# Kernel optimization log

Measured on AMD Instinct MI355X. Metric: run time of the kernel, lower is better.

Reference implementation:

```python
import jax, jax.numpy as jnp
import numpy as np

B, C, N = 8, 256, 4096
CQK = C // 4  # 64
BN_EPS = 1e-5


def setup_inputs() -> dict:
    key = jax.random.key(0)
    ks = jax.random.split(key, 10)
    s = 1.0 / np.sqrt(C)
    return {
        "x": jax.random.normal(ks[0], (B, C, N), jnp.float32),
        "xyz": jax.random.normal(ks[1], (B, C, N), jnp.float32),
        # q_conv and k_conv share the same weight/bias in the original module
        "wqk": jax.random.uniform(ks[2], (CQK, C), jnp.float32, -s, s),
        "bqk": jax.random.uniform(ks[3], (CQK,), jnp.float32, -s, s),
        "wv": jax.random.uniform(ks[4], (C, C), jnp.float32, -s, s),
        "bv": jax.random.uniform(ks[5], (C,), jnp.float32, -s, s),
        "wt": jax.random.uniform(ks[6], (C, C), jnp.float32, -s, s),
        "bt": jax.random.uniform(ks[7], (C,), jnp.float32, -s, s),
        "bn_gamma": jnp.ones((C,), jnp.float32),
        "bn_beta": jnp.zeros((C,), jnp.float32),
        "bn_mean": jax.random.normal(ks[8], (C,), jnp.float32) * 0.1,
        "bn_var": jax.random.uniform(ks[9], (C,), jnp.float32, 0.5, 1.5),
    }


def _conv1x1(x, w, b):
    # x: [B, Cin, N], w: [Cout, Cin], b: [Cout] -> [B, Cout, N]
    return jnp.einsum('oc,bcn->bon', w, x) + b[None, :, None]


def reference(x, xyz, wqk, bqk, wv, bv, wt, bt, bn_gamma, bn_beta, bn_mean, bn_var):
    x = x + xyz
    q = _conv1x1(x, wqk, bqk)            # [B, 64, N]
    k = _conv1x1(x, wqk, bqk)            # [B, 64, N] (shared weights)
    v = _conv1x1(x, wv, bv)              # [B, C, N]
    energy = jnp.einsum('bci,bcj->bij', q, k)   # q^T k -> [B, N, N]
    attn = jax.nn.softmax(energy, axis=-1)
    attn = attn / (1e-9 + attn.sum(axis=1, keepdims=True))  # L1 column renorm
    x_r = jnp.einsum('bcn,bnm->bcm', v, attn)    # [B, C, N]
    t = _conv1x1(x - x_r, wt, bt)
    # BatchNorm1d (eval mode, running stats)
    inv = jax.lax.rsqrt(bn_var + BN_EPS)
    t = (t - bn_mean[None, :, None]) * (inv * bn_gamma)[None, :, None] + bn_beta[None, :, None]
    x_r = jnp.where(t >= 0, t, 0.2 * t)          # LeakyReLU(0.2)
    return x + x_r
```

## Files before the change

### kernel.cpp

```cpp
#include <hip/hip_runtime.h>
#include <math.h>

#define B_   8
#define C_   256
#define N_   4096
#define CQK_ 64
#define JS_  8
#define NSPLIT 2
#define NRANGE (N_ / NSPLIT)

#define SCQ 1.20110674f
#define THR2 11.54f

typedef __attribute__((ext_vector_type(8))) short short8v;
typedef __attribute__((ext_vector_type(4))) short short4v;
typedef __attribute__((ext_vector_type(4))) float f32x4;
typedef __attribute__((ext_vector_type(16))) float f32x16;
typedef __attribute__((ext_vector_type(4))) unsigned int uint4v;

__device__ __forceinline__ unsigned short f2bf(float f) {
    unsigned u = __float_as_uint(f);
    u += 0x7fffu + ((u >> 16) & 1u);
    return (unsigned short)(u >> 16);
}
__device__ __forceinline__ float bf2f(unsigned short h) {
    return __uint_as_float((unsigned)h << 16);
}
__device__ __forceinline__ float fexp2(float x) { return __builtin_amdgcn_exp2f(x); }


__global__ __launch_bounds__(256) void wcvt_kernel(const float* __restrict__ wqk,
                                                   const float* __restrict__ wv,
                                                   const float* __restrict__ wt,
                                                   unsigned short* __restrict__ wh) {
    int i = (blockIdx.x * 256 + threadIdx.x) * 4;
    const float* src; int off;
    if (i < 16384)      { src = wqk; off = i; }
    else if (i < 81920) { src = wv;  off = i - 16384; }
    else                { src = wt;  off = i - 81920; }
    float4 v = *(const float4*)(src + off);
    short4v o;
    o[0] = (short)f2bf(v.x); o[1] = (short)f2bf(v.y);
    o[2] = (short)f2bf(v.z); o[3] = (short)f2bf(v.w);
    *(short4v*)(wh + i) = o;
}

__global__ __launch_bounds__(256) void addt_kernel(const float* __restrict__ x,
                                                   const float* __restrict__ xyz,
                                                   float* __restrict__ xs,
                                                   unsigned short* __restrict__ xst) {
    __shared__ float st[64][65];
    const int tid = threadIdx.x;
    const int n0 = blockIdx.x * 64, c0 = blockIdx.y * 64, b = blockIdx.z;
    const size_t base = ((size_t)b * C_ + c0) * N_ + n0;
#pragma unroll
    for (int r = 0; r < 4; ++r) {
        int c = r * 16 + (tid >> 4);
        int nc = (tid & 15) * 4;
        size_t off = base + (size_t)c * N_ + nc;
        float4 xv = *(const float4*)(x + off);
        float4 yv = *(const float4*)(xyz + off);
        float4 s = make_float4(xv.x + yv.x, xv.y + yv.y, xv.z + yv.z, xv.w + yv.w);
        *(float4*)(xs + off) = s;
        st[c][nc] = s.x; st[c][nc + 1] = s.y; st[c][nc + 2] = s.z; st[c][nc + 3] = s.w;
    }
    __syncthreads();
    int n = tid >> 2, cc = (tid & 3) * 16;
    short8v p0, p1;
#pragma unroll
    for (int j = 0; j < 8; ++j) {
        p0[j] = (short)f2bf(st[cc + j][n]);
        p1[j] = (short)f2bf(st[cc + 8 + j][n]);
    }
    size_t ob = ((size_t)b * N_ + n0 + n) * 256 + c0 + cc;
    *(short8v*)(xst + ob) = p0;
    *(short8v*)(xst + ob + 8) = p1;
}

__global__ __launch_bounds__(256, 4) void convq_kernel(const unsigned short* __restrict__ xst,
                                                       const unsigned short* __restrict__ wh,
                                                       const float* __restrict__ bias,
                                                       unsigned short* __restrict__ Qf) {
    const int tid = threadIdx.x, wave = tid >> 6, lane = tid & 63, q = lane & 15, g = lane >> 4;
    const int n0 = blockIdx.x * 64, b = blockIdx.y;
    const unsigned short* xb = xst + (size_t)b * N_ * 256;
    f32x4 acc[4];
#pragma unroll
    for (int j = 0; j < 4; ++j) acc[j] = (f32x4){0.f, 0.f, 0.f, 0.f};
    for (int ks = 0; ks < 8; ++ks) {
        short8v aw = *(const short8v*)(wh + (size_t)(wave * 16 + q) * 256 + ks * 32 + 8 * g);
#pragma unroll
        for (int j = 0; j < 4; ++j) {
            short8v bx = *(const short8v*)(xb + (size_t)(n0 + j * 16 + q) * 256 + ks * 32 + 8 * g);
            acc[j] = __builtin_amdgcn_mfma_f32_16x16x32_bf16(aw, bx, acc[j], 0, 0, 0);
        }
    }
#pragma unroll
    for (int j = 0; j < 4; ++j) {
        short4v pk;
#pragma unroll
        for (int r = 0; r < 4; ++r)
            pk[r] = (short)f2bf((acc[j][r] + bias[wave * 16 + 4 * g + r]) * SCQ);
        const int n = n0 + j * 16 + q;
        size_t a = ((((size_t)b * 128 + (n >> 5)) * 4 + wave) * 64 + (g >> 1) * 32 + (n & 31)) * 8
                   + (g & 1) * 4;
        *(short4v*)(Qf + a) = pk;
    }
}

__global__ __launch_bounds__(512, 2) void convv_kernel(const unsigned short* __restrict__ xst,
                                                       const unsigned short* __restrict__ wh,
                                                       const float* __restrict__ bias,
                                                       const float* __restrict__ rsinv,
                                                       unsigned short* __restrict__ Vf) {
    const int tid = threadIdx.x, wave = tid >> 6, lane = tid & 63, q = lane & 15, g = lane >> 4;
    const int n0 = blockIdx.x * 64, o0 = blockIdx.y * 128, b = blockIdx.z;
    const int oo = o0 + wave * 16;
    const unsigned short* xb = xst + (size_t)b * N_ * 256;
    const float* rsb = rsinv + (size_t)b * N_;
    f32x4 acc[4];
#pragma unroll
    for (int j = 0; j < 4; ++j) acc[j] = (f32x4){0.f, 0.f, 0.f, 0.f};
    for (int ks = 0; ks < 8; ++ks) {
        short8v bw = *(const short8v*)(wh + (size_t)(oo + q) * 256 + ks * 32 + 8 * g);
#pragma unroll
        for (int j = 0; j < 4; ++j) {
            short8v ax = *(const short8v*)(xb + (size_t)(n0 + j * 16 + q) * 256 + ks * 32 + 8 * g);
            acc[j] = __builtin_amdgcn_mfma_f32_16x16x32_bf16(ax, bw, acc[j], 0, 0, 0);
        }
    }
    float bo = bias[oo + q];
    const int c = oo + q;
#pragma unroll
    for (int j = 0; j < 4; ++j) {
        f32x4 rs4 = *(const f32x4*)(rsb + n0 + j * 16 + 4 * g);
        short4v pk;
#pragma unroll
        for (int r = 0; r < 4; ++r) pk[r] = (short)f2bf((acc[j][r] + bo) * rs4[r]);
        size_t a = ((((size_t)b * 256 + (n0 >> 4) + j) * 8 + (c >> 5)) * 64
                    + (g >> 1) * 32 + (c & 31)) * 8 + (g & 1) * 4;
        *(short4v*)(Vf + a) = pk;
    }
}

__global__ __launch_bounds__(256) void rowstats_mfma(const unsigned short* __restrict__ Qf,
                                                     float* __restrict__ pmax,
                                                     float* __restrict__ psum) {
    const int tid = threadIdx.x;
    const int wave = tid >> 6, lane = tid & 63, l31 = lane & 31;
    const int bid = blockIdx.x;
    const int b  = bid & 7;
    const int it = (bid >> 3) & 31;
    const int js = bid >> 8;
    const int i0 = it * 128 + wave * 32;
    const unsigned short* Qb = Qf + (size_t)b * 128 * 4 * 512;

    short8v bqi[4];
#pragma unroll
    for (int ks = 0; ks < 4; ++ks)
        bqi[ks] = *(const short8v*)(Qb + (((size_t)(i0 >> 5) * 4 + ks) * 64 + lane) * 8);

    float m = -1e30f, s = 0.f;
    const int jbeg = js * (N_ / JS_);
    for (int j0 = jbeg; j0 < jbeg + N_ / JS_; j0 += 32) {
        short8v an[4];
#pragma unroll
        for (int ks = 0; ks < 4; ++ks)
            an[ks] = *(const short8v*)(Qb + (((size_t)(j0 >> 5) * 4 + ks) * 64 + lane) * 8);
        f32x16 e;
#pragma unroll
        for (int r = 0; r < 16; ++r) e[r] = 0.f;
#pragma unroll
        for (int ks = 0; ks < 4; ++ks)
            e = __builtin_amdgcn_mfma_f32_32x32x16_bf16(an[ks], bqi[ks], e, 0, 0, 0);
        float pm = e[0];
#pragma unroll
        for (int r = 1; r < 16; ++r) pm = fmaxf(pm, e[r]);
        if (!__all(pm <= m + THR2)) {
            float mn = fmaxf(m, pm);
            s *= fexp2(m - mn);
            m = mn;
        }
#pragma unroll
        for (int r = 0; r < 16; ++r) s += fexp2(e[r] - m);
    }
    {
        float mo = __shfl_xor(m, 32);
        float so = __shfl_xor(s, 32);
        float mn = fmaxf(m, mo);
        s = s * fexp2(m - mn) + so * fexp2(mo - mn);
        m = mn;
    }
    if (lane < 32) {
        size_t o = ((size_t)js * B_ + b) * N_ + i0 + l31;
        pmax[o] = m;
        psum[o] = s;
    }
}

__global__ __launch_bounds__(256) void rowmerge_kernel(const float* __restrict__ pmax,
                                                       const float* __restrict__ psum,
                                                       float* __restrict__ rmneg,
                                                       float* __restrict__ rsinv) {
    size_t i = (size_t)blockIdx.x * 256 + threadIdx.x;
    float m = -1e30f;
#pragma unroll
    for (int js = 0; js < JS_; ++js) m = fmaxf(m, pmax[(size_t)js * B_ * N_ + i]);
    float s = 0.f;
#pragma unroll
    for (int js = 0; js < JS_; ++js)
        s += psum[(size_t)js * B_ * N_ + i] * fexp2(pmax[(size_t)js * B_ * N_ + i] - m);
    rmneg[i] = -m;
    rsinv[i] = 1.f / s;
}

__global__ __launch_bounds__(256, 2) void pv_mfma32(const unsigned short* __restrict__ Qf,
                                                    const unsigned short* __restrict__ Vf,
                                                    const float* __restrict__ rmneg,
                                                    const float* __restrict__ rsinv,
                                                    unsigned short* __restrict__ pxr,
                                                    float* __restrict__ pcs) {
    const int tid = threadIdx.x;
    const int wave = tid >> 6, lane = tid & 63, l31 = lane & 31, hi = lane >> 5;
    const int bid = blockIdx.x;
    const int b  = bid & 7;
    const int mc = (bid >> 3) & 31;
    const int ns = bid >> 8;
    const int m0 = mc * 128 + wave * 32;
    const int nbeg = ns * NRANGE;
    const unsigned short* Qb = Qf + (size_t)b * 128 * 4 * 512;
    const unsigned short* Vb = Vf + (size_t)b * 256 * 8 * 512;
    const float* rmb = rmneg + (size_t)b * N_;
    const float* rsb = rsinv + (size_t)b * N_;

    short8v bqm[4];
#pragma unroll
    for (int ks = 0; ks < 4; ++ks)
        bqm[ks] = *(const short8v*)(Qb + (((size_t)(m0 >> 5) * 4 + ks) * 64 + lane) * 8);

    f32x16 acc[8];
#pragma unroll
    for (int cb = 0; cb < 8; ++cb)
#pragma unroll
        for (int r = 0; r < 16; ++r) acc[cb][r] = 0.f;
    f32x4 csum4 = {0.f, 0.f, 0.f, 0.f};

#pragma unroll 1
    for (int it = 0; it < NRANGE / 32; ++it) {
        const int n0 = nbeg + it * 32;
        const int nt = n0 >> 5;
        short8v an[4];
#pragma unroll
        for (int ks = 0; ks < 4; ++ks)
            an[ks] = *(const short8v*)(Qb + (((size_t)nt * 4 + ks) * 64 + lane) * 8);
        f32x4 rmn[4], rs[4];
#pragma unroll
        for (int s = 0; s < 4; ++s) {
            rmn[s] = *(const f32x4*)(rmb + n0 + 8 * s + 4 * hi);
            rs[s]  = *(const f32x4*)(rsb + n0 + 8 * s + 4 * hi);
        }
        f32x16 e;
#pragma unroll
        for (int s = 0; s < 4; ++s) {
            e[4 * s + 0] = rmn[s][0]; e[4 * s + 1] = rmn[s][1];
            e[4 * s + 2] = rmn[s][2]; e[4 * s + 3] = rmn[s][3];
        }
#pragma unroll
        for (int ks = 0; ks < 4; ++ks)
            e = __builtin_amdgcn_mfma_f32_32x32x16_bf16(an[ks], bqm[ks], e, 0, 0, 0);
        unsigned dw[8];
#pragma unroll
        for (int s = 0; s < 4; ++s) {
            float p0 = fexp2(e[4 * s + 0]);
            float p1 = fexp2(e[4 * s + 1]);
            float p2 = fexp2(e[4 * s + 2]);
            float p3 = fexp2(e[4 * s + 3]);
            csum4[s] += (p0 * rs[s][0] + p1 * rs[s][1]) + (p2 * rs[s][2] + p3 * rs[s][3]);
            asm("v_cvt_pk_bf16_f32 %0, %1, %2" : "=v"(dw[2 * s + 0]) : "v"(p0), "v"(p1));
            asm("v_cvt_pk_bf16_f32 %0, %1, %2" : "=v"(dw[2 * s + 1]) : "v"(p2), "v"(p3));
        }
        asm("v_permlane32_swap_b32 %0, %1" : "+v"(dw[0]), "+v"(dw[2]));
        asm("v_permlane32_swap_b32 %0, %1" : "+v"(dw[1]), "+v"(dw[3]));
        asm("v_permlane32_swap_b32 %0, %1" : "+v"(dw[4]), "+v"(dw[6]));
        asm("v_permlane32_swap_b32 %0, %1" : "+v"(dw[5]), "+v"(dw[7]));
        uint4v t0 = {dw[0], dw[1], dw[2], dw[3]};
        uint4v t1 = {dw[4], dw[5], dw[6], dw[7]};
        short8v pf0 = __builtin_bit_cast(short8v, t0);
        short8v pf1 = __builtin_bit_cast(short8v, t1);
        const size_t vb0 = (size_t)(nt * 2) * 8;
#pragma unroll
        for (int cb = 0; cb < 8; ++cb) {
            short8v v0 = *(const short8v*)(Vb + ((vb0 + cb) * 64 + lane) * 8);
            acc[cb] = __builtin_amdgcn_mfma_f32_32x32x16_bf16(v0, pf0, acc[cb], 0, 0, 0);
        }
#pragma unroll
        for (int cb = 0; cb < 8; ++cb) {
            short8v v1 = *(const short8v*)(Vb + ((vb0 + 8 + cb) * 64 + lane) * 8);
            acc[cb] = __builtin_amdgcn_mfma_f32_32x32x16_bf16(v1, pf1, acc[cb], 0, 0, 0);
        }
    }

    float csum = (csum4[0] + csum4[1]) + (csum4[2] + csum4[3]);
    csum += __shfl_xor(csum, 32);
    if (lane < 32) pcs[((size_t)ns * B_ + b) * N_ + m0 + lane] = csum;
    unsigned short* pb = pxr + ((size_t)ns * B_ + b) * N_ * 256;
    const int m = m0 + l31;
#pragma unroll
    for (int cb = 0; cb < 8; ++cb)
#pragma unroll
        for (int s = 0; s < 4; ++s) {
            short4v pk;
#pragma unroll
            for (int r = 0; r < 4; ++r) pk[r] = (short)f2bf(acc[cb][4 * s + r]);
            *(short4v*)(pb + (size_t)m * 256 + cb * 32 + 8 * s + 4 * hi) = pk;
        }
}

__global__ __launch_bounds__(256) void reduce_diff(const unsigned short* __restrict__ pxr,
                                                   const float* __restrict__ pcs,
                                                   unsigned short* __restrict__ dh) {
    size_t i = (size_t)blockIdx.x * 256 + threadIdx.x;
    size_t e0 = i * 8;
    int m = (int)((e0 >> 8) & (N_ - 1));
    int b = (int)(e0 >> 20);
    float cs = pcs[(size_t)b * N_ + m] + pcs[((size_t)B_ + b) * N_ + m];
    float inv = 1.f / (1e-9f + cs);
    short8v p0 = *(const short8v*)(pxr + e0);
    short8v p1 = *(const short8v*)(pxr + (size_t)B_ * N_ * 256 + e0);
    short8v xv = *(const short8v*)(dh + e0);
    short8v o;
#pragma unroll
    for (int j = 0; j < 8; ++j) {
        float xr = (bf2f((unsigned short)p0[j]) + bf2f((unsigned short)p1[j])) * inv;
        o[j] = (short)f2bf(bf2f((unsigned short)xv[j]) - xr);
    }
    *(short8v*)(dh + e0) = o;
}

__global__ __launch_bounds__(512, 2) void convt_kernel(const unsigned short* __restrict__ dh,
                                                       const unsigned short* __restrict__ wh,
                                                       const float* __restrict__ bt,
                                                       const float* __restrict__ xs,
                                                       float* __restrict__ out,
                                                       const float* __restrict__ gam,
                                                       const float* __restrict__ bet,
                                                       const float* __restrict__ mu,
                                                       const float* __restrict__ var) {
    const int tid = threadIdx.x, wave = tid >> 6, lane = tid & 63, q = lane & 15, g = lane >> 4;
    const int m0 = blockIdx.x * 64, c0 = blockIdx.y * 128, b = blockIdx.z;
    const int cc = c0 + wave * 16;
    const unsigned short* db = dh + (size_t)b * N_ * 256;
    f32x4 acc[4];
#pragma unroll
    for (int j = 0; j < 4; ++j) acc[j] = (f32x4){0.f, 0.f, 0.f, 0.f};
    for (int ks = 0; ks < 8; ++ks) {
        short8v bw = *(const short8v*)(wh + (size_t)(cc + q) * 256 + ks * 32 + 8 * g);
#pragma unroll
        for (int j = 0; j < 4; ++j) {
            short8v ad = *(const short8v*)(db + (size_t)(m0 + j * 16 + q) * 256 + ks * 32 + 8 * g);
            acc[j] = __builtin_amdgcn_mfma_f32_16x16x32_bf16(ad, bw, acc[j], 0, 0, 0);
        }
    }
    const int c = cc + q;
    const float sc = rsqrtf(var[c] + 1e-5f) * gam[c];
    const float sh = bet[c] - mu[c] * sc;
    const float bb = bt[c];
#pragma unroll
    for (int j = 0; j < 4; ++j) {
        size_t off = ((size_t)b * C_ + c) * N_ + m0 + j * 16 + 4 * g;
        float4 xv = *(const float4*)(xs + off);
        float4 o;
        float tn;
        tn = (acc[j][0] + bb) * sc + sh; o.x = xv.x + (tn >= 0.f ? tn : 0.2f * tn);
        tn = (acc[j][1] + bb) * sc + sh; o.y = xv.y + (tn >= 0.f ? tn : 0.2f * tn);
        tn = (acc[j][2] + bb) * sc + sh; o.z = xv.z + (tn >= 0.f ? tn : 0.2f * tn);
        tn = (acc[j][3] + bb) * sc + sh; o.w = xv.w + (tn >= 0.f ? tn : 0.2f * tn);
        *(float4*)(out + off) = o;
    }
}

extern "C" void kernel_launch(void* const* d_in, const int* in_sizes, int n_in,
                              void* d_out, int out_size, void* d_ws, size_t ws_size,
                              hipStream_t stream) {
    (void)in_sizes; (void)n_in; (void)out_size; (void)ws_size;
    const float* x   = (const float*)d_in[0];
    const float* xyz = (const float*)d_in[1];
    const float* wqk = (const float*)d_in[2];
    const float* bqk = (const float*)d_in[3];
    const float* wv  = (const float*)d_in[4];
    const float* bv  = (const float*)d_in[5];
    const float* wt  = (const float*)d_in[6];
    const float* bt  = (const float*)d_in[7];
    const float* gam = (const float*)d_in[8];
    const float* bet = (const float*)d_in[9];
    const float* mu  = (const float*)d_in[10];
    const float* var = (const float*)d_in[11];
    float* out = (float*)d_out;

    const size_t M8 = (size_t)B_ * C_ * N_;
    float* ws = (float*)d_ws;
    size_t off = 0;
    float* xs = ws + off;                              off += M8;
    unsigned short* xst = (unsigned short*)(ws + off); off += M8 / 2;
    unsigned short* Qf  = (unsigned short*)(ws + off); off += M8 / 8;
    unsigned short* Vf  = (unsigned short*)(ws + off); off += M8 / 2;
    unsigned short* wh  = (unsigned short*)(ws + off); off += 81920;
    float* pmax = ws + off; off += (size_t)JS_ * B_ * N_;
    float* psum = ws + off; off += (size_t)JS_ * B_ * N_;
    float* rmb  = ws + off; off += (size_t)B_ * N_;
    float* rsb  = ws + off; off += (size_t)B_ * N_;
    float* pcs  = ws + off; off += (size_t)NSPLIT * B_ * N_;
    unsigned short* pxr = (unsigned short*)(ws + off); off += M8;
    unsigned short* dhb = xst;

    wcvt_kernel<<<dim3(144), dim3(256), 0, stream>>>(wqk, wv, wt, wh);
    addt_kernel<<<dim3(N_ / 64, C_ / 64, B_), dim3(256), 0, stream>>>(x, xyz, xs, xst);
    convq_kernel<<<dim3(N_ / 64, B_), dim3(256), 0, stream>>>(xst, wh, bqk, Qf);
    rowstats_mfma<<<dim3(B_ * 32 * JS_), dim3(256), 0, stream>>>(Qf, pmax, psum);
    rowmerge_kernel<<<dim3(B_ * N_ / 256), dim3(256), 0, stream>>>(pmax, psum, rmb, rsb);
    convv_kernel<<<dim3(N_ / 64, C_ / 128, B_), dim3(512), 0, stream>>>(
        xst, wh + 16384, bv, rsb, Vf);
    pv_mfma32<<<dim3(B_ * 32 * NSPLIT), dim3(256), 0, stream>>>(Qf, Vf, rmb, rsb, pxr, pcs);
    reduce_diff<<<dim3(B_ * N_ * C_ / 8 / 256), dim3(256), 0, stream>>>(pxr, pcs, dhb);
    convt_kernel<<<dim3(N_ / 64, C_ / 128, B_), dim3(512), 0, stream>>>(
        dhb, wh + 81920, bt, xs, out, gam, bet, mu, var);
}
```

Baseline: 303.2 us.

## Share P tiles across waves via LDS so each wave loads only its V slice

In the PV kernel, each wave previously computed its own 32-row P block and multiplied it against all 256 channels of V, so every wave streamed the full V tile from global memory. Now each wave writes its P fragments to double-buffered shared memory. After a block barrier, each wave loads only the 64-channel V slice it owns and multiplies it against all four waves' P blocks. This cuts global V traffic per block by a factor of four. In exchange it adds LDS writes and reads plus a __syncthreads in every iteration of the inner loop.

```diff
diff --git a/kernel.cpp b/kernel.cpp
--- a/kernel.cpp
+++ b/kernel.cpp
@@ -220,13 +220,14 @@
                                                     const float* __restrict__ rsinv,
                                                     unsigned short* __restrict__ pxr,
                                                     float* __restrict__ pcs) {
+    __shared__ unsigned short Pl[2][4][2][64][8];
     const int tid = threadIdx.x;
     const int wave = tid >> 6, lane = tid & 63, l31 = lane & 31, hi = lane >> 5;
     const int bid = blockIdx.x;
     const int b  = bid & 7;
     const int mc = (bid >> 3) & 31;
     const int ns = bid >> 8;
-    const int m0 = mc * 128 + wave * 32;
+    const int m0 = mc * 128;
     const int nbeg = ns * NRANGE;
     const unsigned short* Qb = Qf + (size_t)b * 128 * 4 * 512;
     const unsigned short* Vb = Vf + (size_t)b * 256 * 8 * 512;
@@ -236,19 +237,22 @@
     short8v bqm[4];
 #pragma unroll
     for (int ks = 0; ks < 4; ++ks)
-        bqm[ks] = *(const short8v*)(Qb + (((size_t)(m0 >> 5) * 4 + ks) * 64 + lane) * 8);
-
-    f32x16 acc[8];
-#pragma unroll
-    for (int cb = 0; cb < 8; ++cb)
-#pragma unroll
-        for (int r = 0; r < 16; ++r) acc[cb][r] = 0.f;
+        bqm[ks] = *(const short8v*)(Qb + (((size_t)((m0 >> 5) + wave) * 4 + ks) * 64 + lane) * 8);
+
+    f32x16 acc[4][2];
+#pragma unroll
+    for (int mk = 0; mk < 4; ++mk)
+#pragma unroll
+        for (int cb = 0; cb < 2; ++cb)
+#pragma unroll
+            for (int r = 0; r < 16; ++r) acc[mk][cb][r] = 0.f;
     f32x4 csum4 = {0.f, 0.f, 0.f, 0.f};
 
 #pragma unroll 1
     for (int it = 0; it < NRANGE / 32; ++it) {
         const int n0 = nbeg + it * 32;
         const int nt = n0 >> 5;
+        const int cur = it & 1;
         short8v an[4];
 #pragma unroll
         for (int ks = 0; ks < 4; ++ks)
@@ -285,35 +289,40 @@
         asm("v_permlane32_swap_b32 %0, %1" : "+v"(dw[5]), "+v"(dw[7]));
         uint4v t0 = {dw[0], dw[1], dw[2], dw[3]};
         uint4v t1 = {dw[4], dw[5], dw[6], dw[7]};
-        short8v pf0 = __builtin_bit_cast(short8v, t0);
-        short8v pf1 = __builtin_bit_cast(short8v, t1);
+        *(uint4v*)&Pl[cur][wave][0][lane][0] = t0;
+        *(uint4v*)&Pl[cur][wave][1][lane][0] = t1;
+        __syncthreads();
         const size_t vb0 = (size_t)(nt * 2) * 8;
 #pragma unroll
-        for (int cb = 0; cb < 8; ++cb) {
-            short8v v0 = *(const short8v*)(Vb + ((vb0 + cb) * 64 + lane) * 8);
-            acc[cb] = __builtin_amdgcn_mfma_f32_32x32x16_bf16(v0, pf0, acc[cb], 0, 0, 0);
-        }
-#pragma unroll
-        for (int cb = 0; cb < 8; ++cb) {
-            short8v v1 = *(const short8v*)(Vb + ((vb0 + 8 + cb) * 64 + lane) * 8);
-            acc[cb] = __builtin_amdgcn_mfma_f32_32x32x16_bf16(v1, pf1, acc[cb], 0, 0, 0);
+        for (int nh = 0; nh < 2; ++nh) {
+            short8v v0 = *(const short8v*)(Vb + ((vb0 + nh * 8 + wave * 2 + 0) * 64 + lane) * 8);
+            short8v v1 = *(const short8v*)(Vb + ((vb0 + nh * 8 + wave * 2 + 1) * 64 + lane) * 8);
+#pragma unroll
+            for (int mk = 0; mk < 4; ++mk) {
+                short8v pf = *(const short8v*)&Pl[cur][mk][nh][lane][0];
+                acc[mk][0] = __builtin_amdgcn_mfma_f32_32x32x16_bf16(v0, pf, acc[mk][0], 0, 0, 0);
+                acc[mk][1] = __builtin_amdgcn_mfma_f32_32x32x16_bf16(v1, pf, acc[mk][1], 0, 0, 0);
+            }
         }
     }
 
     float csum = (csum4[0] + csum4[1]) + (csum4[2] + csum4[3]);
     csum += __shfl_xor(csum, 32);
-    if (lane < 32) pcs[((size_t)ns * B_ + b) * N_ + m0 + lane] = csum;
+    if (lane < 32) pcs[((size_t)ns * B_ + b) * N_ + m0 + wave * 32 + l31] = csum;
     unsigned short* pb = pxr + ((size_t)ns * B_ + b) * N_ * 256;
-    const int m = m0 + l31;
-#pragma unroll
-    for (int cb = 0; cb < 8; ++cb)
-#pragma unroll
-        for (int s = 0; s < 4; ++s) {
-            short4v pk;
-#pragma unroll
-            for (int r = 0; r < 4; ++r) pk[r] = (short)f2bf(acc[cb][4 * s + r]);
-            *(short4v*)(pb + (size_t)m * 256 + cb * 32 + 8 * s + 4 * hi) = pk;
-        }
+#pragma unroll
+    for (int mk = 0; mk < 4; ++mk) {
+        const int m = m0 + mk * 32 + l31;
+#pragma unroll
+        for (int cb = 0; cb < 2; ++cb)
+#pragma unroll
+            for (int s = 0; s < 4; ++s) {
+                short4v pk;
+#pragma unroll
+                for (int r = 0; r < 4; ++r) pk[r] = (short)f2bf(acc[mk][cb][4 * s + r]);
+                *(short4v*)(pb + (size_t)m * 256 + (wave * 2 + cb) * 32 + 8 * s + 4 * hi) = pk;
+            }
+    }
 }
 
 __global__ __launch_bounds__(256) void reduce_diff(const unsigned short* __restrict__ pxr,
```

After: 280.4 us. -7.5%, faster.
